# Kernel tuning notes

Measured on AMD Instinct MI355X. Metric: run time of the kernel, lower is better.

## Reference

```python
import jax, jax.numpy as jnp
import numpy as np

D_MODEL = 1024
NUM_HEADS = 16
HEAD_DIM = D_MODEL // NUM_HEADS  # 64
M_BITS = 32
B, N = 4, 2048


def setup_inputs() -> dict:
    key = jax.random.key(0)
    ks = jax.random.split(key, 6)
    s = 1.0 / np.sqrt(D_MODEL)
    se = 1.0 / np.sqrt(HEAD_DIM)
    return {
        "x": jax.random.normal(ks[0], (B, N, D_MODEL), dtype=jnp.float32),
        "Wq": jax.random.normal(ks[1], (D_MODEL, D_MODEL), dtype=jnp.float32) * s,
        "Wk": jax.random.normal(ks[2], (D_MODEL, D_MODEL), dtype=jnp.float32) * s,
        "Wv": jax.random.normal(ks[3], (D_MODEL, D_MODEL), dtype=jnp.float32) * s,
        # per-head witness (bit) encoders: project head_dim -> m_bits
        "W_enc": jax.random.normal(ks[4], (NUM_HEADS, HEAD_DIM, M_BITS), dtype=jnp.float32) * se,
        "Wo": jax.random.normal(ks[5], (D_MODEL, D_MODEL), dtype=jnp.float32) * s,
    }


def reference(x, Wq, Wk, Wv, W_enc, Wo):
    Bsz, Nq, _ = x.shape
    # QKV projections (nn.Linear, no bias): y = x @ W^T
    Q = x @ Wq.T
    K = x @ Wk.T  # self-attention: context = x
    V = x @ Wv.T
    # split heads: [B, N, H, hd]
    Qh = Q.reshape(Bsz, Nq, NUM_HEADS, HEAD_DIM)
    Kh = K.reshape(Bsz, Nq, NUM_HEADS, HEAD_DIM)
    Vh = V.reshape(Bsz, Nq, NUM_HEADS, HEAD_DIM)
    # witness encodings: soft-bit (tanh of random-hyperplane projections), m_bits << head_dim feature space
    q_enc = jnp.tanh(jnp.einsum("bnhd,hdm->bnhm", Qh, W_enc))
    k_enc = jnp.tanh(jnp.einsum("bnhd,hdm->bnhm", Kh, W_enc))
    # witness similarity scores over m_bits instead of full head_dim
    scale = 1.0 / np.sqrt(M_BITS)
    scores = jnp.einsum("bnhm,bkhm->bhnk", q_enc, k_enc) * scale  # [B,H,N,N]
    attn = jax.nn.softmax(scores, axis=-1)
    out = jnp.einsum("bhnk,bkhd->bnhd", attn, Vh).reshape(Bsz, Nq, D_MODEL)
    return out @ Wo.T
```

## Files before the change

kernel.cpp:

```cpp
#include <hip/hip_runtime.h>

typedef unsigned short u16;
typedef unsigned int u32;

typedef __bf16 bfrag __attribute__((ext_vector_type(8)));
typedef float f32x4 __attribute__((ext_vector_type(4)));
typedef float f32x16 __attribute__((ext_vector_type(16)));
typedef float f32x2 __attribute__((ext_vector_type(2)));

__device__ __forceinline__ float b2f(u16 h) {
    u32 u = ((u32)h) << 16;
    return __builtin_bit_cast(float, u);
}
__device__ __forceinline__ u16 f2b(float f) {
    u32 u = __builtin_bit_cast(u32, f);
    u += 0x7fffu + ((u >> 16) & 1u);
    return (u16)(u >> 16);
}
__device__ __forceinline__ u32 cvtpk(float lo, float hi) {
    u32 r;
    asm("v_cvt_pk_bf16_f32 %0, %1, %2" : "=v"(r) : "v"(lo), "v"(hi));
    return r;
}

#if defined(__has_builtin)
#if __has_builtin(__builtin_amdgcn_exp2f)
#define EXP2(x) __builtin_amdgcn_exp2f(x)
#endif
#endif
#ifndef EXP2
#define EXP2(x) exp2f(x)
#endif

#if defined(__has_builtin)
#if __has_builtin(__builtin_amdgcn_global_load_lds)
#define HAS_GLL 1
#endif
#endif
#ifndef HAS_GLL
#define HAS_GLL 0
#endif

#if HAS_GLL
typedef __attribute__((address_space(1))) const u32 as1_u32;
typedef __attribute__((address_space(3))) u32 as3_u32;
__device__ __forceinline__ void gl_lds16(const u16* g, u16* l) {
    __builtin_amdgcn_global_load_lds((as1_u32*)g, (as3_u32*)l, 16, 0, 0);
}
#endif

#if defined(__has_builtin)
#if __has_builtin(__builtin_amdgcn_permlane32_swap)
#define HAS_PLS 1
#endif
#endif
#ifndef HAS_PLS
#define HAS_PLS 0
#endif

__device__ __forceinline__ void plswap(u32 a, u32 b, u32& o0, u32& o1) {
#if HAS_PLS
    auto r = __builtin_amdgcn_permlane32_swap((int)a, (int)b, false, false);
    o0 = (u32)r[0];
    o1 = (u32)r[1];
#else
    int idx = ((int)(threadIdx.x & 63) ^ 32) << 2;
    u32 ca = (u32)__builtin_amdgcn_ds_bpermute(idx, (int)a);
    u32 cb = (u32)__builtin_amdgcn_ds_bpermute(idx, (int)b);
    bool hi = (threadIdx.x & 63) >= 32;
    o0 = hi ? cb : a;
    o1 = hi ? b : ca;
#endif
}

__device__ __forceinline__ void xcd_swizzle(int& bxn, int& bym) {
    int gx = gridDim.x;
    int nwg = gx * gridDim.y;
    int orig = blockIdx.x + gx * blockIdx.y;
    int nid = orig;
    if ((nwg & 7) == 0) {
        int cpx = nwg >> 3;
        nid = (orig & 7) * cpx + (orig >> 3);
    }
    bxn = nid % gx;
    bym = nid / gx;
}

#define BATCH 4
#define SEQ   2048
#define DM    1024
#define NH    16
#define HD    64
#define MB    32
#define STOK  (BATCH * SEQ)

#define QSCALE 0.25503524337503433f
#define TWOLOG2E 2.8853900817779268f

__device__ __forceinline__ void storeC(u16* C, size_t idx, float v)   { C[idx] = f2b(v); }
__device__ __forceinline__ void storeC(float* C, size_t idx, float v) { C[idx] = v; }

__global__ __launch_bounds__(256) void cvt_f32_bf16(
    const float* __restrict__ s, u16* __restrict__ d, int n8)
{
    int i = blockIdx.x * 256 + threadIdx.x;
    if (i >= n8) return;
    const float4* sp = (const float4*)s + (size_t)i * 2;
    float4 a = sp[0], b = sp[1];
    u16 t[8] = { f2b(a.x), f2b(a.y), f2b(a.z), f2b(a.w),
                 f2b(b.x), f2b(b.y), f2b(b.z), f2b(b.w) };
    ((uint4*)d)[i] = *(uint4*)t;
}

__global__ __launch_bounds__(256) void cvt2_f32_bf16(
    const float* __restrict__ a, const float* __restrict__ b,
    u16* __restrict__ da, u16* __restrict__ db, int n8)
{
    const float* s = blockIdx.y ? b : a;
    u16* d = blockIdx.y ? db : da;
    int i = blockIdx.x * 256 + threadIdx.x;
    if (i >= n8) return;
    const float4* sp = (const float4*)s + (size_t)i * 2;
    float4 x = sp[0], y = sp[1];
    u16 t[8] = { f2b(x.x), f2b(x.y), f2b(x.z), f2b(x.w),
                 f2b(y.x), f2b(y.y), f2b(y.z), f2b(y.w) };
    ((uint4*)d)[i] = *(uint4*)t;
}

__global__ __launch_bounds__(256) void build_cqk(
    const float* __restrict__ Wq, const float* __restrict__ Wk,
    const float* __restrict__ Wenc, u16* __restrict__ CqkT)
{
    const int dblk = blockIdx.x;
    const int qk   = blockIdx.y >> 4;
    const int h    = blockIdx.y & 15;
    const float* W = qk ? Wk : Wq;
    __shared__ float we[64][32];
    const int tid = threadIdx.x;

    for (int p = 0; p < 8; ++p) {
        int idx = p * 256 + tid;
        we[idx >> 5][idx & 31] = Wenc[(size_t)h * (HD * MB) + idx];
    }
    __syncthreads();

    const int mh = tid >> 7;
    const int d  = dblk * 128 + (tid & 127);
    float acc[16] = {};
    for (int dh = 0; dh < 64; ++dh) {
        float w = W[(size_t)(h * 64 + dh) * DM + d];
        for (int m = 0; m < 16; ++m)
            acc[m] += w * we[dh][mh * 16 + m];
    }
    u16* dst = CqkT + (size_t)(qk * 512 + h * 32 + mh * 16) * DM + d;
    for (int m = 0; m < 16; ++m)
        dst[(size_t)m * DM] = f2b(acc[m]);
}

template <int TBM, typename TC>
__global__ __launch_bounds__(256) void gemm_bt(
    const u16* __restrict__ A, const u16* __restrict__ Bt, TC* __restrict__ C,
    int M, int Nc, int K)
{
    constexpr int FI = TBM / 32;
    __shared__ alignas(16) u16 As[TBM * 32];
    __shared__ alignas(16) u16 Bs[128 * 32];

    const int tid  = threadIdx.x;
    const int wave = tid >> 6;
    const int lane = tid & 63;
    const int quad = lane >> 4;
    const int lrow = lane & 15;
    int bxn, bym;
    xcd_swizzle(bxn, bym);
    const int bm = bym * TBM;
    const int bn = bxn * 128;
    const int wm = (wave & 1) * (TBM / 2);
    const int wn = (wave >> 1) * 64;

    f32x4 acc[FI][4] = {};

    for (int k0 = 0; k0 < K; k0 += 32) {
#if HAS_GLL
        for (int p = 0; p < TBM / 64; ++p) {
            int cbase = wave * TBM + p * 64;
            int cme   = cbase + lane;
            int row = cme >> 2, col = (cme & 3) * 8;
            gl_lds16(&A[(size_t)(bm + row) * K + k0 + col], &As[(size_t)cbase * 8]);
        }
        for (int p = 0; p < 2; ++p) {
            int cbase = wave * 128 + p * 64;
            int cme   = cbase + lane;
            int row = cme >> 2, col = (cme & 3) * 8;
            gl_lds16(&Bt[(size_t)(bn + row) * K + k0 + col], &Bs[(size_t)cbase * 8]);
        }
#else
        for (int p = 0; p < TBM / 64; ++p) {
            int idx = p * 256 + tid, row = idx >> 2, col = (idx & 3) * 8;
            *(uint4*)&As[row * 32 + col] = *(const uint4*)&A[(size_t)(bm + row) * K + k0 + col];
        }
        for (int p = 0; p < 2; ++p) {
            int idx = p * 256 + tid, row = idx >> 2, col = (idx & 3) * 8;
            *(uint4*)&Bs[row * 32 + col] = *(const uint4*)&Bt[(size_t)(bn + row) * K + k0 + col];
        }
#endif
        __syncthreads();

        bfrag af[FI], bfv[4];
        for (int i = 0; i < FI; ++i)
            af[i] = *(const bfrag*)&As[(wm + i * 16 + lrow) * 32 + quad * 8];
        for (int j = 0; j < 4; ++j)
            bfv[j] = *(const bfrag*)&Bs[(wn + j * 16 + lrow) * 32 + quad * 8];

        for (int i = 0; i < FI; ++i)
            for (int j = 0; j < 4; ++j)
                acc[i][j] = __builtin_amdgcn_mfma_f32_16x16x32_bf16(af[i], bfv[j], acc[i][j], 0, 0, 0);
        __syncthreads();
    }

    for (int i = 0; i < FI; ++i)
        for (int j = 0; j < 4; ++j)
            for (int r = 0; r < 4; ++r) {
                int row = bm + wm + i * 16 + quad * 4 + r;
                int col = bn + wn + j * 16 + lrow;
                storeC(C, (size_t)row * Nc + col, acc[i][j][r]);
            }
}

__global__ __launch_bounds__(256) void gemm_encv(
    const u16* __restrict__ A, const u16* __restrict__ Bt,
    u16* __restrict__ qe, u16* __restrict__ ke, u16* __restrict__ Vt)
{
    __shared__ alignas(16) u16 As[128 * 32];
    __shared__ alignas(16) u16 Bs[128 * 32];

    const int tid  = threadIdx.x;
    const int wave = tid >> 6;
    const int lane = tid & 63;
    const int quad = lane >> 4;
    const int lrow = lane & 15;
    int bxn, bym;
    xcd_swizzle(bxn, bym);
    const int bm = bym * 128;
    const int bn = bxn * 128;
    const int wm = (wave & 1) * 64;
    const int wn = (wave >> 1) * 64;

    f32x4 acc[4][4] = {};

    for (int k0 = 0; k0 < DM; k0 += 32) {
#if HAS_GLL
        for (int p = 0; p < 2; ++p) {
            int cbase = wave * 128 + p * 64;
            int cme   = cbase + lane;
            int row = cme >> 2, col = (cme & 3) * 8;
            gl_lds16(&A[(size_t)(bm + row) * DM + k0 + col], &As[(size_t)cbase * 8]);
            gl_lds16(&Bt[(size_t)(bn + row) * DM + k0 + col], &Bs[(size_t)cbase * 8]);
        }
#else
        for (int p = 0; p < 2; ++p) {
            int idx = p * 256 + tid, row = idx >> 2, col = (idx & 3) * 8;
            *(uint4*)&As[row * 32 + col] = *(const uint4*)&A[(size_t)(bm + row) * DM + k0 + col];
            *(uint4*)&Bs[row * 32 + col] = *(const uint4*)&Bt[(size_t)(bn + row) * DM + k0 + col];
        }
#endif
        __syncthreads();

        bfrag af[4], bfv[4];
        for (int i = 0; i < 4; ++i)
            af[i] = *(const bfrag*)&As[(wm + i * 16 + lrow) * 32 + quad * 8];
        for (int j = 0; j < 4; ++j)
            bfv[j] = *(const bfrag*)&Bs[(wn + j * 16 + lrow) * 32 + quad * 8];

        for (int i = 0; i < 4; ++i)
            for (int j = 0; j < 4; ++j)
                acc[i][j] = __builtin_amdgcn_mfma_f32_16x16x32_bf16(af[i], bfv[j], acc[i][j], 0, 0, 0);
        __syncthreads();
    }

    if (bn < 1024) {
        for (int i = 0; i < 4; ++i)
            for (int j = 0; j < 4; ++j) {
                int col = bn + wn + j * 16 + lrow;
                int hh = (col >> 5) & 15;
                int mm = col & 31;
                u16* dst = (col < 512) ? qe : ke;
                float qs = (col < 512) ? QSCALE : 1.0f;
                for (int r = 0; r < 4; ++r) {
                    int row = bm + wm + i * 16 + quad * 4 + r;
                    int bb = row >> 11, nn = row & 2047;
                    float e = EXP2(acc[i][j][r] * TWOLOG2E);
                    float t = (1.f - 2.f / (e + 1.f)) * qs;
                    dst[((size_t)(bb * NH + hh) * SEQ + nn) * MB + mm] = f2b(t);
                }
            }
    } else {
        for (int i = 0; i < 4; ++i)
            for (int j = 0; j < 4; ++j) {
                int col = bn - 1024 + wn + j * 16 + lrow;
                int hh = col >> 6, dd = col & 63;
                int row0 = bm + wm + i * 16 + quad * 4;
                int bb = row0 >> 11, nn = row0 & 2047;
                u16 t4[4] = { f2b(acc[i][j][0]), f2b(acc[i][j][1]),
                              f2b(acc[i][j][2]), f2b(acc[i][j][3]) };
                *(uint2*)&Vt[((size_t)(bb * NH + hh) * HD + dd) * SEQ + nn] = *(uint2*)t4;
            }
    }
}

__global__ __launch_bounds__(256, 4) void flash_attn(
    const u16* __restrict__ qe,
    const u16* __restrict__ ke,
    const u16* __restrict__ Vt,
    u16* __restrict__ AO)
{
    const int h = blockIdx.x, b = blockIdx.y, qt = blockIdx.z;
    const int tid  = threadIdx.x;
    const int wave = tid >> 6;
    const int lane = tid & 63;
    const int r31  = lane & 31;
    const int hi   = lane >> 5;

    __shared__ alignas(16) u16 Kt[2][64 * 32];
    __shared__ alignas(16) u16 Vtile[2][64 * 64];

    const size_t bhh = (size_t)(b * NH + h);
    const u16* keb = ke + bhh * SEQ * MB;
    const u16* qeb = qe + bhh * SEQ * MB;
    const u16* vtb = Vt + bhh * HD * SEQ;

    const int q0w = qt * 128 + wave * 32;

    const int klr = tid >> 2;
    const int ksl = tid & 3;
    const u16* ksrc = keb + (size_t)klr * MB + ((ksl ^ (klr & 3)) * 8);
    const int d0 = wave * 8 + (lane >> 3);
    const int c0 = lane & 7;
    const int g0 = (c0 ^ (d0 & 7)) * 8;
    const u16* vsrc0 = vtb + (size_t)d0 * SEQ + g0;
    const u16* vsrc1 = vtb + (size_t)(d0 + 32) * SEQ + g0;

#if HAS_GLL
    gl_lds16(ksrc,  Kt[0] + wave * 512);
    gl_lds16(vsrc0, Vtile[0] + wave * 512);
    gl_lds16(vsrc1, Vtile[0] + 2048 + wave * 512);
#else
    *(uint4*)&Kt[0][klr * 32 + ksl * 8] = *(const uint4*)ksrc;
    *(uint4*)&Vtile[0][d0 * 64 + c0 * 8] = *(const uint4*)vsrc0;
    *(uint4*)&Vtile[0][(d0 + 32) * 64 + c0 * 8] = *(const uint4*)vsrc1;
#endif
    ksrc += 64 * MB;
    vsrc0 += 64;
    vsrc1 += 64;

    bfrag qf[2];
    {
        const u16* qrow = qeb + (size_t)(q0w + r31) * MB;
        qf[0] = *(const bfrag*)&qrow[hi * 8];
        qf[1] = *(const bfrag*)&qrow[16 + hi * 8];
    }

    const f32x16 zero16 = {};

    f32x16 Oa[2] = {};
    f32x2 dacc = {0.f, 0.f};
    const int ksw = r31 & 3;
    const int vsw = r31 & 7;

    for (int c = 0; c < 32; ++c) {
        const int cur = c & 1, nxt = cur ^ 1;
        __syncthreads();

        if (c + 1 < 32) {
#if HAS_GLL
            gl_lds16(ksrc,  Kt[nxt] + wave * 512);
            gl_lds16(vsrc0, Vtile[nxt] + wave * 512);
            gl_lds16(vsrc1, Vtile[nxt] + 2048 + wave * 512);
#else
            *(uint4*)&Kt[nxt][klr * 32 + ksl * 8] = *(const uint4*)ksrc;
            *(uint4*)&Vtile[nxt][d0 * 64 + c0 * 8] = *(const uint4*)vsrc0;
            *(uint4*)&Vtile[nxt][(d0 + 32) * 64 + c0 * 8] = *(const uint4*)vsrc1;
#endif
            ksrc += 64 * MB;
            vsrc0 += 64;
            vsrc1 += 64;
        }

        const u16* KtC = Kt[cur];
        const u16* VtC = Vtile[cur];

        bfrag kf[2][2];
        for (int kt = 0; kt < 2; ++kt) {
            const u16* krow = &KtC[(kt * 32 + r31) * 32];
            kf[kt][0] = *(const bfrag*)&krow[((hi    ) ^ ksw) * 8];
            kf[kt][1] = *(const bfrag*)&krow[((2 + hi) ^ ksw) * 8];
        }

        bfrag pf[2][2];
        for (int kt = 0; kt < 2; ++kt) {
            __builtin_amdgcn_s_setprio(1);
            f32x16 St = __builtin_amdgcn_mfma_f32_32x32x16_bf16(kf[kt][0], qf[0], zero16, 0, 0, 0);
            St = __builtin_amdgcn_mfma_f32_32x32x16_bf16(kf[kt][1], qf[1], St, 0, 0, 0);
            __builtin_amdgcn_s_setprio(0);
            for (int kc = 0; kc < 2; ++kc) {
                float e0 = EXP2(St[8 * kc + 0]);
                float e1 = EXP2(St[8 * kc + 1]);
                float e2 = EXP2(St[8 * kc + 2]);
                float e3 = EXP2(St[8 * kc + 3]);
                float e4 = EXP2(St[8 * kc + 4]);
                float e5 = EXP2(St[8 * kc + 5]);
                float e6 = EXP2(St[8 * kc + 6]);
                float e7 = EXP2(St[8 * kc + 7]);
                f32x2 p0 = {e0, e1}, p1 = {e2, e3}, p2 = {e4, e5}, p3 = {e6, e7};
                dacc += (p0 + p1) + (p2 + p3);
                u32 A0 = cvtpk(e0, e1), A1 = cvtpk(e2, e3);
                u32 B0 = cvtpk(e4, e5), B1 = cvtpk(e6, e7);
                u32 w0, w1, w2, w3;
                plswap(A0, B0, w0, w2);
                plswap(A1, B1, w1, w3);
                uint4 words = { w0, w1, w2, w3 };
                pf[kt][kc] = __builtin_bit_cast(bfrag, words);
            }
        }

        __builtin_amdgcn_s_setprio(1);
        for (int dt = 0; dt < 2; ++dt) {
            const u16* vrow = &VtC[(dt * 32 + r31) * 64];
            for (int kt = 0; kt < 2; ++kt)
                for (int kc = 0; kc < 2; ++kc) {
                    bfrag vf = *(const bfrag*)&vrow[(((kt * 4 + kc * 2 + hi) ^ vsw) * 8)];
                    Oa[dt] = __builtin_amdgcn_mfma_f32_32x32x16_bf16(vf, pf[kt][kc], Oa[dt], 0, 0, 0);
                }
        }
        __builtin_amdgcn_s_setprio(0);
    }

    float dsum = dacc[0] + dacc[1];
    u32 o0, o1;
    plswap(__builtin_bit_cast(u32, dsum), __builtin_bit_cast(u32, dsum), o0, o1);
    float den = __builtin_bit_cast(float, o0) + __builtin_bit_cast(float, o1);

    {
        float inv = 1.0f / den;
        u16* aob = AO + (size_t)(b * SEQ + q0w + r31) * DM + h * HD;
        for (int dt = 0; dt < 2; ++dt)
            for (int g = 0; g < 4; ++g) {
                u16 t4[4] = { f2b(Oa[dt][g * 4 + 0] * inv),
                              f2b(Oa[dt][g * 4 + 1] * inv),
                              f2b(Oa[dt][g * 4 + 2] * inv),
                              f2b(Oa[dt][g * 4 + 3] * inv) };
                *(uint2*)&aob[dt * 32 + g * 8 + hi * 4] = *(uint2*)t4;
            }
    }
}

extern "C" void kernel_launch(void* const* d_in, const int* in_sizes, int n_in,
                              void* d_out, int out_size, void* d_ws, size_t ws_size,
                              hipStream_t stream) {
    const float* x    = (const float*)d_in[0];
    const float* Wq   = (const float*)d_in[1];
    const float* Wk   = (const float*)d_in[2];
    const float* Wv   = (const float*)d_in[3];
    const float* Wenc = (const float*)d_in[4];
    const float* Wo   = (const float*)d_in[5];
    float* out = (float*)d_out;

    const size_t MB1 = (size_t)1024 * 1024;
    char* ws = (char*)d_ws;
    u16* AO   = (u16*)(ws);
    u16* Wo_b = (u16*)(ws + 16 * MB1);
    u16* Bc   = (u16*)(ws + 18 * MB1);
    u16* Vt   = (u16*)(ws + 24 * MB1);
    u16* qe   = (u16*)(ws + 48 * MB1);
    u16* ke   = (u16*)(ws + 56 * MB1);

    u16* xb = (u16*)d_out;
    u16* wvb = Bc + (size_t)1024 * DM;

    cvt_f32_bf16<<<dim3(STOK * DM / 8 / 256), 256, 0, stream>>>(x, xb, STOK * DM / 8);
    cvt2_f32_bf16<<<dim3(DM * DM / 8 / 256, 2), 256, 0, stream>>>(Wv, Wo, wvb, Wo_b, DM * DM / 8);
    build_cqk<<<dim3(8, 32), 256, 0, stream>>>(Wq, Wk, Wenc, Bc);

    gemm_encv<<<dim3(2048 / 128, STOK / 128), 256, 0, stream>>>(xb, Bc, qe, ke, Vt);

    flash_attn<<<dim3(NH, BATCH, SEQ / 128), 256, 0, stream>>>(qe, ke, Vt, AO);

    gemm_bt<64, float><<<dim3(DM / 128, STOK / 64), 256, 0, stream>>>(AO, Wo_b, out, STOK, DM, DM);
}
```

Baseline: 258.8 us.

## Load K fragments directly to registers, unroll attention loop, merge conversion kernels

The flash attention kernel stops staging K tiles through shared memory. Each lane now loads its K fragments straight from global memory into registers, double-buffered across a manually unrolled two-step loop, while V still goes through LDS double buffering. The x, Wv and Wo fp32-to-bf16 conversions are merged into one launch, which saves a launch but leaves most blocks in the weight jobs exiting early. The direct K loads cut LDS traffic and shared memory use, at the cost of more registers and global load latency that is exposed to the MFMA pipeline.

```diff
diff --git a/kernel.cpp b/kernel.cpp
--- a/kernel.cpp
+++ b/kernel.cpp
@@ -100,24 +100,16 @@
 __device__ __forceinline__ void storeC(u16* C, size_t idx, float v)   { C[idx] = f2b(v); }
 __device__ __forceinline__ void storeC(float* C, size_t idx, float v) { C[idx] = v; }
 
-__global__ __launch_bounds__(256) void cvt_f32_bf16(
-    const float* __restrict__ s, u16* __restrict__ d, int n8)
-{
-    int i = blockIdx.x * 256 + threadIdx.x;
-    if (i >= n8) return;
-    const float4* sp = (const float4*)s + (size_t)i * 2;
-    float4 a = sp[0], b = sp[1];
-    u16 t[8] = { f2b(a.x), f2b(a.y), f2b(a.z), f2b(a.w),
-                 f2b(b.x), f2b(b.y), f2b(b.z), f2b(b.w) };
-    ((uint4*)d)[i] = *(uint4*)t;
-}
-
-__global__ __launch_bounds__(256) void cvt2_f32_bf16(
+__global__ __launch_bounds__(256) void cvt3_f32_bf16(
     const float* __restrict__ a, const float* __restrict__ b,
-    u16* __restrict__ da, u16* __restrict__ db, int n8)
-{
-    const float* s = blockIdx.y ? b : a;
-    u16* d = blockIdx.y ? db : da;
+    const float* __restrict__ c,
+    u16* __restrict__ da, u16* __restrict__ db, u16* __restrict__ dc,
+    int n8a, int n8bc)
+{
+    const int job = blockIdx.y;
+    const float* s = (job == 0) ? a : ((job == 1) ? b : c);
+    u16* d = (job == 0) ? da : ((job == 1) ? db : dc);
+    int n8 = (job == 0) ? n8a : n8bc;
     int i = blockIdx.x * 256 + threadIdx.x;
     if (i >= n8) return;
     const float4* sp = (const float4*)s + (size_t)i * 2;
@@ -308,6 +300,70 @@
     }
 }
 
+__device__ __forceinline__ bfrag pack_half(const f32x16& St, int kc, f32x2& dacc)
+{
+    float e0 = EXP2(St[8 * kc + 0]);
+    float e1 = EXP2(St[8 * kc + 1]);
+    float e2 = EXP2(St[8 * kc + 2]);
+    float e3 = EXP2(St[8 * kc + 3]);
+    float e4 = EXP2(St[8 * kc + 4]);
+    float e5 = EXP2(St[8 * kc + 5]);
+    float e6 = EXP2(St[8 * kc + 6]);
+    float e7 = EXP2(St[8 * kc + 7]);
+    f32x2 p0 = {e0, e1}, p1 = {e2, e3}, p2 = {e4, e5}, p3 = {e6, e7};
+    dacc += (p0 + p1) + (p2 + p3);
+    u32 A0 = cvtpk(e0, e1), A1 = cvtpk(e2, e3);
+    u32 B0 = cvtpk(e4, e5), B1 = cvtpk(e6, e7);
+    u32 w0, w1, w2, w3;
+    plswap(A0, B0, w0, w2);
+    plswap(A1, B1, w1, w3);
+    uint4 words = { w0, w1, w2, w3 };
+    return __builtin_bit_cast(bfrag, words);
+}
+
+__device__ __forceinline__ void fa_step(
+    bfrag k00, bfrag k01, bfrag k10, bfrag k11,
+    bfrag qf0, bfrag qf1, const u16* __restrict__ VtC,
+    int vsw, int r31, int hi,
+    f32x16& Oa0, f32x16& Oa1, f32x2& dacc)
+{
+    const f32x16 zero16 = {};
+    bfrag pf[2][2];
+
+    __builtin_amdgcn_s_setprio(1);
+    f32x16 St0 = __builtin_amdgcn_mfma_f32_32x32x16_bf16(k00, qf0, zero16, 0, 0, 0);
+    St0 = __builtin_amdgcn_mfma_f32_32x32x16_bf16(k01, qf1, St0, 0, 0, 0);
+    __builtin_amdgcn_s_setprio(0);
+    pf[0][0] = pack_half(St0, 0, dacc);
+    pf[0][1] = pack_half(St0, 1, dacc);
+
+    __builtin_amdgcn_s_setprio(1);
+    f32x16 St1 = __builtin_amdgcn_mfma_f32_32x32x16_bf16(k10, qf0, zero16, 0, 0, 0);
+    St1 = __builtin_amdgcn_mfma_f32_32x32x16_bf16(k11, qf1, St1, 0, 0, 0);
+    __builtin_amdgcn_s_setprio(0);
+    pf[1][0] = pack_half(St1, 0, dacc);
+    pf[1][1] = pack_half(St1, 1, dacc);
+
+    __builtin_amdgcn_s_setprio(1);
+    const u16* vrow0 = &VtC[(size_t)r31 * 64];
+    const u16* vrow1 = &VtC[(size_t)(32 + r31) * 64];
+    for (int kt = 0; kt < 2; ++kt)
+        for (int kc = 0; kc < 2; ++kc) {
+            int ch = ((kt * 4 + kc * 2 + hi) ^ vsw) * 8;
+            bfrag vf0 = *(const bfrag*)&vrow0[ch];
+            Oa0 = __builtin_amdgcn_mfma_f32_32x32x16_bf16(vf0, pf[kt][kc], Oa0, 0, 0, 0);
+            bfrag vf1 = *(const bfrag*)&vrow1[ch];
+            Oa1 = __builtin_amdgcn_mfma_f32_32x32x16_bf16(vf1, pf[kt][kc], Oa1, 0, 0, 0);
+        }
+    __builtin_amdgcn_s_setprio(0);
+}
+
+#define K_LD(p, a0, a1, a2, a3) do { \
+    a0 = *(const bfrag*)(p); \
+    a1 = *(const bfrag*)((p) + 16); \
+    a2 = *(const bfrag*)((p) + 32 * MB); \
+    a3 = *(const bfrag*)((p) + 32 * MB + 16); } while (0)
+
 __global__ __launch_bounds__(256, 4) void flash_attn(
     const u16* __restrict__ qe,
     const u16* __restrict__ ke,
@@ -321,7 +377,6 @@
     const int r31  = lane & 31;
     const int hi   = lane >> 5;
 
-    __shared__ alignas(16) u16 Kt[2][64 * 32];
     __shared__ alignas(16) u16 Vtile[2][64 * 64];
 
     const size_t bhh = (size_t)(b * NH + h);
@@ -331,9 +386,6 @@
 
     const int q0w = qt * 128 + wave * 32;
 
-    const int klr = tid >> 2;
-    const int ksl = tid & 3;
-    const u16* ksrc = keb + (size_t)klr * MB + ((ksl ^ (klr & 3)) * 8);
     const int d0 = wave * 8 + (lane >> 3);
     const int c0 = lane & 7;
     const int g0 = (c0 ^ (d0 & 7)) * 8;
@@ -341,98 +393,64 @@
     const u16* vsrc1 = vtb + (size_t)(d0 + 32) * SEQ + g0;
 
 #if HAS_GLL
-    gl_lds16(ksrc,  Kt[0] + wave * 512);
     gl_lds16(vsrc0, Vtile[0] + wave * 512);
     gl_lds16(vsrc1, Vtile[0] + 2048 + wave * 512);
 #else
-    *(uint4*)&Kt[0][klr * 32 + ksl * 8] = *(const uint4*)ksrc;
     *(uint4*)&Vtile[0][d0 * 64 + c0 * 8] = *(const uint4*)vsrc0;
     *(uint4*)&Vtile[0][(d0 + 32) * 64 + c0 * 8] = *(const uint4*)vsrc1;
 #endif
-    ksrc += 64 * MB;
     vsrc0 += 64;
     vsrc1 += 64;
 
-    bfrag qf[2];
+    const u16* kp = keb + (size_t)r31 * MB + hi * 8;
+    bfrag kA0, kA1, kA2, kA3;
+    bfrag kB0, kB1, kB2, kB3;
+    K_LD(kp, kA0, kA1, kA2, kA3);
+    kp += 64 * MB;
+
+    bfrag qf0, qf1;
     {
         const u16* qrow = qeb + (size_t)(q0w + r31) * MB;
-        qf[0] = *(const bfrag*)&qrow[hi * 8];
-        qf[1] = *(const bfrag*)&qrow[16 + hi * 8];
-    }
-
-    const f32x16 zero16 = {};
-
-    f32x16 Oa[2] = {};
+        qf0 = *(const bfrag*)&qrow[hi * 8];
+        qf1 = *(const bfrag*)&qrow[16 + hi * 8];
+    }
+
+    f32x16 Oa0 = {}, Oa1 = {};
     f32x2 dacc = {0.f, 0.f};
-    const int ksw = r31 & 3;
     const int vsw = r31 & 7;
 
-    for (int c = 0; c < 32; ++c) {
-        const int cur = c & 1, nxt = cur ^ 1;
+    for (int c = 0; c < 32; c += 2) {
         __syncthreads();
-
-        if (c + 1 < 32) {
+        {
 #if HAS_GLL
-            gl_lds16(ksrc,  Kt[nxt] + wave * 512);
-            gl_lds16(vsrc0, Vtile[nxt] + wave * 512);
-            gl_lds16(vsrc1, Vtile[nxt] + 2048 + wave * 512);
+            gl_lds16(vsrc0, Vtile[1] + wave * 512);
+            gl_lds16(vsrc1, Vtile[1] + 2048 + wave * 512);
 #else
-            *(uint4*)&Kt[nxt][klr * 32 + ksl * 8] = *(const uint4*)ksrc;
-            *(uint4*)&Vtile[nxt][d0 * 64 + c0 * 8] = *(const uint4*)vsrc0;
-            *(uint4*)&Vtile[nxt][(d0 + 32) * 64 + c0 * 8] = *(const uint4*)vsrc1;
-#endif
-            ksrc += 64 * MB;
+            *(uint4*)&Vtile[1][d0 * 64 + c0 * 8] = *(const uint4*)vsrc0;
+            *(uint4*)&Vtile[1][(d0 + 32) * 64 + c0 * 8] = *(const uint4*)vsrc1;
+#endif
             vsrc0 += 64;
             vsrc1 += 64;
-        }
-
-        const u16* KtC = Kt[cur];
-        const u16* VtC = Vtile[cur];
-
-        bfrag kf[2][2];
-        for (int kt = 0; kt < 2; ++kt) {
-            const u16* krow = &KtC[(kt * 32 + r31) * 32];
-            kf[kt][0] = *(const bfrag*)&krow[((hi    ) ^ ksw) * 8];
-            kf[kt][1] = *(const bfrag*)&krow[((2 + hi) ^ ksw) * 8];
-        }
-
-        bfrag pf[2][2];
-        for (int kt = 0; kt < 2; ++kt) {
-            __builtin_amdgcn_s_setprio(1);
-            f32x16 St = __builtin_amdgcn_mfma_f32_32x32x16_bf16(kf[kt][0], qf[0], zero16, 0, 0, 0);
-            St = __builtin_amdgcn_mfma_f32_32x32x16_bf16(kf[kt][1], qf[1], St, 0, 0, 0);
-            __builtin_amdgcn_s_setprio(0);
-            for (int kc = 0; kc < 2; ++kc) {
-                float e0 = EXP2(St[8 * kc + 0]);
-                float e1 = EXP2(St[8 * kc + 1]);
-                float e2 = EXP2(St[8 * kc + 2]);
-                float e3 = EXP2(St[8 * kc + 3]);
-                float e4 = EXP2(St[8 * kc + 4]);
-                float e5 = EXP2(St[8 * kc + 5]);
-                float e6 = EXP2(St[8 * kc + 6]);
-                float e7 = EXP2(St[8 * kc + 7]);
-                f32x2 p0 = {e0, e1}, p1 = {e2, e3}, p2 = {e4, e5}, p3 = {e6, e7};
-                dacc += (p0 + p1) + (p2 + p3);
-                u32 A0 = cvtpk(e0, e1), A1 = cvtpk(e2, e3);
-                u32 B0 = cvtpk(e4, e5), B1 = cvtpk(e6, e7);
-                u32 w0, w1, w2, w3;
-                plswap(A0, B0, w0, w2);
-                plswap(A1, B1, w1, w3);
-                uint4 words = { w0, w1, w2, w3 };
-                pf[kt][kc] = __builtin_bit_cast(bfrag, words);
-            }
-        }
-
-        __builtin_amdgcn_s_setprio(1);
-        for (int dt = 0; dt < 2; ++dt) {
-            const u16* vrow = &VtC[(dt * 32 + r31) * 64];
-            for (int kt = 0; kt < 2; ++kt)
-                for (int kc = 0; kc < 2; ++kc) {
-                    bfrag vf = *(const bfrag*)&vrow[(((kt * 4 + kc * 2 + hi) ^ vsw) * 8)];
-                    Oa[dt] = __builtin_amdgcn_mfma_f32_32x32x16_bf16(vf, pf[kt][kc], Oa[dt], 0, 0, 0);
-                }
-        }
-        __builtin_amdgcn_s_setprio(0);
+            K_LD(kp, kB0, kB1, kB2, kB3);
+            kp += 64 * MB;
+        }
+        fa_step(kA0, kA1, kA2, kA3, qf0, qf1, Vtile[0], vsw, r31, hi, Oa0, Oa1, dacc);
+
+        __syncthreads();
+        if (c + 2 < 32) {
+#if HAS_GLL
+            gl_lds16(vsrc0, Vtile[0] + wave * 512);
+            gl_lds16(vsrc1, Vtile[0] + 2048 + wave * 512);
+#else
+            *(uint4*)&Vtile[0][d0 * 64 + c0 * 8] = *(const uint4*)vsrc0;
+            *(uint4*)&Vtile[0][(d0 + 32) * 64 + c0 * 8] = *(const uint4*)vsrc1;
+#endif
+            vsrc0 += 64;
+            vsrc1 += 64;
+            K_LD(kp, kA0, kA1, kA2, kA3);
+            kp += 64 * MB;
+        }
+        fa_step(kB0, kB1, kB2, kB3, qf0, qf1, Vtile[1], vsw, r31, hi, Oa0, Oa1, dacc);
     }
 
     float dsum = dacc[0] + dacc[1];
@@ -443,14 +461,16 @@
     {
         float inv = 1.0f / den;
         u16* aob = AO + (size_t)(b * SEQ + q0w + r31) * DM + h * HD;
-        for (int dt = 0; dt < 2; ++dt)
-            for (int g = 0; g < 4; ++g) {
-                u16 t4[4] = { f2b(Oa[dt][g * 4 + 0] * inv),
-                              f2b(Oa[dt][g * 4 + 1] * inv),
-                              f2b(Oa[dt][g * 4 + 2] * inv),
-                              f2b(Oa[dt][g * 4 + 3] * inv) };
-                *(uint2*)&aob[dt * 32 + g * 8 + hi * 4] = *(uint2*)t4;
-            }
+        for (int g = 0; g < 4; ++g) {
+            u16 t4[4] = { f2b(Oa0[g * 4 + 0] * inv), f2b(Oa0[g * 4 + 1] * inv),
+                          f2b(Oa0[g * 4 + 2] * inv), f2b(Oa0[g * 4 + 3] * inv) };
+            *(uint2*)&aob[g * 8 + hi * 4] = *(uint2*)t4;
+        }
+        for (int g = 0; g < 4; ++g) {
+            u16 t4[4] = { f2b(Oa1[g * 4 + 0] * inv), f2b(Oa1[g * 4 + 1] * inv),
+                          f2b(Oa1[g * 4 + 2] * inv), f2b(Oa1[g * 4 + 3] * inv) };
+            *(uint2*)&aob[32 + g * 8 + hi * 4] = *(uint2*)t4;
+        }
     }
 }
 
@@ -477,8 +497,8 @@
     u16* xb = (u16*)d_out;
     u16* wvb = Bc + (size_t)1024 * DM;
 
-    cvt_f32_bf16<<<dim3(STOK * DM / 8 / 256), 256, 0, stream>>>(x, xb, STOK * DM / 8);
-    cvt2_f32_bf16<<<dim3(DM * DM / 8 / 256, 2), 256, 0, stream>>>(Wv, Wo, wvb, Wo_b, DM * DM / 8);
+    cvt3_f32_bf16<<<dim3(STOK * DM / 8 / 256, 3), 256, 0, stream>>>(
+        x, Wv, Wo, xb, wvb, Wo_b, STOK * DM / 8, DM * DM / 8);
     build_cqk<<<dim3(8, 32), 256, 0, stream>>>(Wq, Wk, Wenc, Bc);
 
     gemm_encv<<<dim3(2048 / 128, STOK / 128), 256, 0, stream>>>(xb, Bc, qe, ke, Vt);
```

New measurement: 262.3 us. About the same (+1.4%).
